# Kernel tuning notes

Measured on AMD Instinct MI355X. Metric: run time of the kernel, lower is better.

The kernel has to match this reference:

```python
import jax, jax.numpy as jnp
import numpy as np

N = 100000   # nodes
E = 3200000  # edges
D = 128      # embedding_dimension


def leaky(x, slope):
    return jnp.where(x >= 0, x, slope * x)


def gat_conv(x, src, dst, lin_w, att_src, att_dst, bias, heads, out_ch):
    """PyG GATConv (concat=True, negative_slope=0.2, add_self_loops handled by caller)."""
    n = x.shape[0]
    h = (x @ lin_w).reshape(n, heads, out_ch)                 # [N,H,C]
    a_s = (h * att_src).sum(-1)                               # [N,H]
    a_d = (h * att_dst).sum(-1)                               # [N,H]
    alpha = leaky(a_s[src] + a_d[dst], 0.2)                   # [E,H]
    # segment softmax over incoming edges of each dst node
    m = jax.ops.segment_max(alpha, dst, num_segments=n)
    ex = jnp.exp(alpha - m[dst])
    s = jax.ops.segment_sum(ex, dst, num_segments=n)
    w = ex / (s[dst] + 1e-16)                                 # [E,H]
    out = jax.ops.segment_sum(h[src] * w[:, :, None], dst, num_segments=n)
    return out.reshape(n, heads * out_ch) + bias


def setup_inputs() -> dict:
    key = jax.random.key(0)
    ks = jax.random.split(key, 32)
    rn = lambda k, s, sc=0.05: jax.random.normal(k, s, dtype=jnp.float32) * sc
    q = D // 4  # 32
    inp = {
        "des": rn(ks[0], (N, 768), 1.0),
        "tweet": rn(ks[1], (N, 768), 1.0),
        "num_prop": rn(ks[2], (N, 6), 1.0),
        "cat_prop": rn(ks[3], (N, 11), 1.0),
        "edge_index": jax.random.randint(ks[4], (2, E), 0, N),
        "edge_type": jax.random.randint(ks[5], (E,), 0, 2),
        # encoder params
        "w_des": rn(ks[6], (768, q)), "b_des": jnp.zeros((q,), jnp.float32),
        "w_tw": rn(ks[7], (768, q)), "b_tw": jnp.zeros((q,), jnp.float32),
        "w_np": rn(ks[8], (6, q)), "b_np": jnp.zeros((q,), jnp.float32),
        "w_cp": rn(ks[9], (11, q)), "b_cp": jnp.zeros((q,), jnp.float32),
        "w_in": rn(ks[10], (D, D)), "b_in": jnp.zeros((D,), jnp.float32),
        # gat1: heads=4, out=32, concat -> 128
        "g1_w": rn(ks[11], (D, 4 * q)), "g1_as": rn(ks[12], (4, q)),
        "g1_ad": rn(ks[13], (4, q)), "g1_b": jnp.zeros((D,), jnp.float32),
        # gat2: heads=1, out=128
        "g2_w": rn(ks[14], (D, D)), "g2_as": rn(ks[15], (1, D)),
        "g2_ad": rn(ks[16], (1, D)), "g2_b": jnp.zeros((D,), jnp.float32),
        # output MLP
        "w_o1": rn(ks[17], (D, D)), "b_o1": jnp.zeros((D,), jnp.float32),
        "w_o2": rn(ks[18], (D, 2)), "b_o2": jnp.zeros((2,), jnp.float32),
    }
    return inp


def reference(des, tweet, num_prop, cat_prop, edge_index, edge_type,
              w_des, b_des, w_tw, b_tw, w_np, b_np, w_cp, b_cp,
              w_in, b_in, g1_w, g1_as, g1_ad, g1_b,
              g2_w, g2_as, g2_ad, g2_b, w_o1, b_o1, w_o2, b_o2):
    # encoders (nn.LeakyReLU default slope = 0.01)
    d = leaky(des @ w_des + b_des, 0.01)
    t = leaky(tweet @ w_tw + b_tw, 0.01)
    n_ = leaky(num_prop @ w_np + b_np, 0.01)
    c = leaky(cat_prop @ w_cp + b_cp, 0.01)
    x = jnp.concatenate([d, t, n_, c], axis=1)          # [N,128]
    x = leaky(x @ w_in + b_in, 0.01)
    # add self-loops (PyG GATConv default add_self_loops=True)
    loop = jnp.arange(N)
    src = jnp.concatenate([edge_index[0], loop])
    dst = jnp.concatenate([edge_index[1], loop])
    x = gat_conv(x, src, dst, g1_w, g1_as, g1_ad, g1_b, 4, D // 4)
    # dropout is identity in eval mode
    x = gat_conv(x, src, dst, g2_w, g2_as, g2_ad, g2_b, 1, D)
    x = leaky(x @ w_o1 + b_o1, 0.01)
    return x @ w_o2 + b_o2                              # [N,2]
```

## Files before the change

kernel.cpp:

```cpp
#include <hip/hip_runtime.h>
#include <hip/hip_bf16.h>

#define DEV_INLINE __device__ __forceinline__

using bf16x8 = __attribute__((ext_vector_type(8))) short;
using f32x4  = __attribute__((ext_vector_type(4))) float;

DEV_INLINE float leaky(float x, float s) { return x >= 0.f ? x : s * x; }
DEV_INLINE float bf2f(unsigned short u) { return __uint_as_float(((unsigned)u) << 16); }
DEV_INLINE unsigned short f2bf(float f) {
  unsigned u = __float_as_uint(f);
  unsigned r = ((u >> 16) & 1u) + 0x7fffu;
  return (unsigned short)((u + r) >> 16);
}
DEV_INLINE float red16(float v) {
  v += __shfl_xor(v, 1, 64); v += __shfl_xor(v, 2, 64);
  v += __shfl_xor(v, 4, 64); v += __shfl_xor(v, 8, 64);
  return v;
}

#define BSHIFT 8
#define NBLK   256

__global__ __launch_bounds__(256) void csr_hist_kernel(
    const int* __restrict__ dst, int* __restrict__ blkcnt, int NB, int E) {
  __shared__ int hist[512];
  int blk = blockIdx.x, t = threadIdx.x;
  for (int i = t; i < NB; i += 256) hist[i] = 0;
  __syncthreads();
  int chunk = (E + NBLK - 1) / NBLK;
  int e0 = blk * chunk;
  int e1 = e0 + chunk; if (e1 > E) e1 = E;
  for (int e = e0 + t; e < e1; e += 256)
    atomicAdd(&hist[dst[e] >> BSHIFT], 1);
  __syncthreads();
  for (int i = t; i < NB; i += 256)
    blkcnt[(size_t)blk * NB + i] = hist[i];
}

__global__ __launch_bounds__(1024) void csr_scan_kernel(
    const int* __restrict__ blkcnt, int* __restrict__ blkoff,
    int* __restrict__ sbkt, int NB) {
  __shared__ int sums[1024];
  int M = NB * NBLK;
  int t = threadIdx.x;
  int chunk = (M + 1023) / 1024;
  int lo = t * chunk;
  int hi = lo + chunk; if (hi > M) hi = M;
  int s = 0;
  for (int q = lo; q < hi; ++q) {
    int b = q >> 8, blk = q & (NBLK - 1);
    s += blkcnt[(size_t)blk * NB + b];
  }
  sums[t] = s;
  __syncthreads();
  for (int off = 1; off < 1024; off <<= 1) {
    int v = (t >= off) ? sums[t - off] : 0;
    __syncthreads();
    sums[t] += v;
    __syncthreads();
  }
  int run = (t == 0) ? 0 : sums[t - 1];
  for (int q = lo; q < hi; ++q) {
    int b = q >> 8, blk = q & (NBLK - 1);
    if (blk == 0) sbkt[b] = run;
    blkoff[(size_t)blk * NB + b] = run;
    run += blkcnt[(size_t)blk * NB + b];
  }
  if (lo < M && hi == M) sbkt[NB] = run;
}

__global__ __launch_bounds__(256) void csr_scatter_kernel(
    const int* __restrict__ src, const int* __restrict__ dst,
    const int* __restrict__ blkoff, int* __restrict__ pairs, int NB, int E) {
  __shared__ int cur[512];
  int blk = blockIdx.x, t = threadIdx.x;
  for (int i = t; i < NB; i += 256) cur[i] = blkoff[(size_t)blk * NB + i];
  __syncthreads();
  int chunk = (E + NBLK - 1) / NBLK;
  int e0 = blk * chunk;
  int e1 = e0 + chunk; if (e1 > E) e1 = E;
  for (int e = e0 + t; e < e1; e += 256) {
    int d = dst[e];
    int pos = atomicAdd(&cur[d >> BSHIFT], 1);
    pairs[pos] = (src[e] << BSHIFT) | (d & 255);
  }
}

__global__ __launch_bounds__(256) void bkt_build_kernel(
    const int* __restrict__ sbkt, const int* __restrict__ pairs,
    int* __restrict__ offs, int* __restrict__ csr, int n_rows, int NB) {
  __shared__ int cnt[256];
  __shared__ int cur[256];
  int b = blockIdx.x, t = threadIdx.x;
  int start = sbkt[b];
  int end   = sbkt[b + 1];
  cnt[t] = 0;
  __syncthreads();
  for (int e = start + t; e < end; e += 256)
    atomicAdd(&cnt[pairs[e] & 255], 1);
  __syncthreads();
  for (int off = 1; off < 256; off <<= 1) {
    int v = (t >= off) ? cnt[t - off] : 0;
    __syncthreads();
    cnt[t] += v;
    __syncthreads();
  }
  int ex = (t == 0) ? 0 : cnt[t - 1];
  cur[t] = start + ex;
  int node = (b << BSHIFT) + t;
  if (node < n_rows) offs[node] = start + ex;
  if (t == 0 && b == NB - 1) offs[n_rows] = end;
  __syncthreads();
  for (int e = start + t; e < end; e += 256) {
    int v = pairs[e];
    int pos = atomicAdd(&cur[v & 255], 1);
    csr[pos] = v >> BSHIFT;
  }
}

__global__ __launch_bounds__(256) void swz_kernel(
    const float* __restrict__ w_des, const float* __restrict__ w_tw,
    const float* __restrict__ w_in, const float* __restrict__ g1_w,
    const float* __restrict__ g2_w, const float* __restrict__ w_o1,
    short* __restrict__ o_des, short* __restrict__ o_tw,
    short* __restrict__ o_in, short* __restrict__ o_g1,
    short* __restrict__ o_g2, short* __restrict__ o_o1) {
  const float* W; short* O; int K, COLS;
  switch (blockIdx.y) {
    case 0: W = w_des; O = o_des; K = 768; COLS = 32; break;
    case 1: W = w_tw;  O = o_tw;  K = 768; COLS = 32; break;
    case 2: W = w_in;  O = o_in;  K = 128; COLS = 128; break;
    case 3: W = g1_w;  O = o_g1;  K = 128; COLS = 128; break;
    case 4: W = g2_w;  O = o_g2;  K = 128; COLS = 128; break;
    default: W = w_o1; O = o_o1;  K = 128; COLS = 128; break;
  }
  int CT = COLS >> 4;
  int t = blockIdx.x * 256 + threadIdx.x;
  int total = (K >> 5) * CT * 64;
  if (t >= total) return;
  int L = t & 63;
  int rest = t >> 6;
  int ct = rest % CT;
  int ks = rest / CT;
  int kbase = ks * 32 + (L >> 4) * 8;
  int col = ct * 16 + (L & 15);
  #pragma unroll
  for (int j = 0; j < 8; ++j)
    O[t * 8 + j] = (short)f2bf(W[(size_t)(kbase + j) * COLS + col]);
}

__global__ __launch_bounds__(256) void enc_mfma_kernel(
    const float* __restrict__ des, const float* __restrict__ tweet,
    const short* __restrict__ wsw_des, const short* __restrict__ wsw_tw,
    const float* __restrict__ b_des, const float* __restrict__ b_tw,
    unsigned short* __restrict__ x0, int n_rows) {
  const float* A; const short* Wsw; const float* bias; int col_off;
  if (blockIdx.y == 0) { A = des;   Wsw = wsw_des; bias = b_des; col_off = 0; }
  else                 { A = tweet; Wsw = wsw_tw;  bias = b_tw;  col_off = 32; }
  int wv = threadIdx.x >> 6, lane = threadIdx.x & 63;
  int row0 = blockIdx.x * 64 + wv * 16;
  int rA = row0 + (lane & 15);
  int rc = rA < n_rows ? rA : (n_rows - 1);
  const float* arow = A + (size_t)rc * 768 + ((lane >> 4) * 8);
  f32x4 acc0 = {0.f, 0.f, 0.f, 0.f}, acc1 = {0.f, 0.f, 0.f, 0.f};

  float4 p0a = *(const float4*)(arow + 0);
  float4 p0b = *(const float4*)(arow + 4);
  float4 p1a = *(const float4*)(arow + 32);
  float4 p1b = *(const float4*)(arow + 36);
  #pragma unroll
  for (int ks = 0; ks < 24; ++ks) {
    float4 c0 = p0a, c1 = p0b;
    p0a = p1a; p0b = p1b;
    if (ks + 2 < 24) {
      p1a = *(const float4*)(arow + (ks + 2) * 32);
      p1b = *(const float4*)(arow + (ks + 2) * 32 + 4);
    }
    bf16x8 af;
    af[0] = (short)f2bf(c0.x); af[1] = (short)f2bf(c0.y);
    af[2] = (short)f2bf(c0.z); af[3] = (short)f2bf(c0.w);
    af[4] = (short)f2bf(c1.x); af[5] = (short)f2bf(c1.y);
    af[6] = (short)f2bf(c1.z); af[7] = (short)f2bf(c1.w);
    bf16x8 b0 = *(const bf16x8*)&Wsw[(size_t)((ks * 2 + 0) * 64 + lane) * 8];
    bf16x8 b1 = *(const bf16x8*)&Wsw[(size_t)((ks * 2 + 1) * 64 + lane) * 8];
    acc0 = __builtin_amdgcn_mfma_f32_16x16x32_bf16(af, b0, acc0, 0, 0, 0);
    acc1 = __builtin_amdgcn_mfma_f32_16x16x32_bf16(af, b1, acc1, 0, 0, 0);
  }
  int quad = lane >> 4, cl = lane & 15;
  #pragma unroll
  for (int r = 0; r < 4; ++r) {
    int row = row0 + quad * 4 + r;
    if (row >= n_rows) continue;
    float v0 = leaky(acc0[r] + bias[cl], 0.01f);
    float v1 = leaky(acc1[r] + bias[16 + cl], 0.01f);
    x0[(size_t)row * 128 + col_off + cl]      = f2bf(v0);
    x0[(size_t)row * 128 + col_off + 16 + cl] = f2bf(v1);
  }
}

__global__ __launch_bounds__(256) void enc_small_kernel(
    const float* __restrict__ np_, const float* __restrict__ cp,
    const float* __restrict__ w_np, const float* __restrict__ w_cp,
    const float* __restrict__ b_np, const float* __restrict__ b_cp,
    unsigned short* __restrict__ x0, int n_rows) {
  int gid = blockIdx.x * 256 + threadIdx.x;
  int node = gid >> 6;
  int c = gid & 63;
  if (node >= n_rows) return;
  float acc; int col;
  if (c < 32) {
    acc = b_np[c];
    #pragma unroll
    for (int k = 0; k < 6; ++k) acc += np_[(size_t)node * 6 + k] * w_np[k * 32 + c];
    col = 64 + c;
  } else {
    int cc = c - 32;
    acc = b_cp[cc];
    #pragma unroll
    for (int k = 0; k < 11; ++k) acc += cp[(size_t)node * 11 + k] * w_cp[k * 32 + cc];
    col = 96 + cc;
  }
  x0[(size_t)node * 128 + col] = f2bf(leaky(acc, 0.01f));
}

__global__ __launch_bounds__(256) void h1_fused_kernel(
    const unsigned short* __restrict__ X, const short* __restrict__ sw_in,
    const float* __restrict__ b_in, const short* __restrict__ sw_g1,
    const float* __restrict__ att_s, const float* __restrict__ att_d,
    unsigned short* __restrict__ H1, float* __restrict__ a_s,
    float* __restrict__ a_d, int n_rows) {
  __shared__ char xt[4 * 4096];
  int wv = threadIdx.x >> 6, lane = threadIdx.x & 63;
  int row0 = blockIdx.x * 64 + wv * 16;
  int rA = row0 + (lane & 15);
  int rc = rA < n_rows ? rA : (n_rows - 1);
  const unsigned short* xr = X + (size_t)rc * 128 + (lane >> 4) * 8;
  int quad = lane >> 4, cl = lane & 15;
  char* xw = xt + wv * 4096;

  f32x4 acc[8] = {};
  #pragma unroll
  for (int ks = 0; ks < 4; ++ks) {
    bf16x8 af = *(const bf16x8*)(xr + ks * 32);
    #pragma unroll
    for (int ct = 0; ct < 8; ++ct) {
      bf16x8 bfr = *(const bf16x8*)&sw_in[(size_t)((ks * 8 + ct) * 64 + lane) * 8];
      acc[ct] = __builtin_amdgcn_mfma_f32_16x16x32_bf16(af, bfr, acc[ct], 0, 0, 0);
    }
  }
  #pragma unroll
  for (int r = 0; r < 4; ++r) {
    int lr = quad * 4 + r;
    #pragma unroll
    for (int ct = 0; ct < 8; ++ct) {
      float v = leaky(acc[ct][r] + b_in[ct * 16 + cl], 0.01f);
      int cb = (ct * 32 + cl * 2) ^ ((lr & 7) << 4);
      *(unsigned short*)(xw + lr * 256 + cb) = f2bf(v);
    }
  }
  f32x4 acc2[8] = {};
  int lr2 = lane & 15;
  #pragma unroll
  for (int ks = 0; ks < 4; ++ks) {
    int cb0 = (((lane >> 4) * 16 + ks * 64)) ^ ((lr2 & 7) << 4);
    bf16x8 af = *(const bf16x8*)(xw + lr2 * 256 + cb0);
    #pragma unroll
    for (int ct = 0; ct < 8; ++ct) {
      bf16x8 bfr = *(const bf16x8*)&sw_g1[(size_t)((ks * 8 + ct) * 64 + lane) * 8];
      acc2[ct] = __builtin_amdgcn_mfma_f32_16x16x32_bf16(af, bfr, acc2[ct], 0, 0, 0);
    }
  }
  float asv[8], adv[8];
  #pragma unroll
  for (int ct = 0; ct < 8; ++ct) {
    int idx = (ct >> 1) * 32 + (ct & 1) * 16 + cl;
    asv[ct] = att_s[idx];
    adv[ct] = att_d[idx];
  }
  #pragma unroll
  for (int r = 0; r < 4; ++r) {
    int row = row0 + quad * 4 + r;
    bool ok = row < n_rows;
    if (ok) {
      #pragma unroll
      for (int ct = 0; ct < 8; ++ct)
        H1[(size_t)row * 128 + ct * 16 + cl] = f2bf(acc2[ct][r]);
    }
    #pragma unroll
    for (int h = 0; h < 4; ++h) {
      float ps = acc2[2 * h][r] * asv[2 * h] + acc2[2 * h + 1][r] * asv[2 * h + 1];
      float pd = acc2[2 * h][r] * adv[2 * h] + acc2[2 * h + 1][r] * adv[2 * h + 1];
      ps = red16(ps); pd = red16(pd);
      if (ok && cl == 0) {
        a_s[(size_t)row * 4 + h] = ps;
        a_d[(size_t)row * 4 + h] = pd;
      }
    }
  }
}

__global__ __launch_bounds__(256) void h2_fused_kernel(
    const unsigned short* __restrict__ X, const short* __restrict__ Wsw,
    const float* __restrict__ att_s, const float* __restrict__ att_d,
    unsigned short* __restrict__ H2, float* __restrict__ a_s,
    float* __restrict__ a_d, int n_rows) {
  int wv = threadIdx.x >> 6, lane = threadIdx.x & 63;
  int row0 = blockIdx.x * 64 + wv * 16;
  int rA = row0 + (lane & 15);
  int rc = rA < n_rows ? rA : (n_rows - 1);
  const unsigned short* xr = X + (size_t)rc * 128 + (lane >> 4) * 8;
  int quad = lane >> 4, cl = lane & 15;
  f32x4 acc[8] = {};
  #pragma unroll
  for (int ks = 0; ks < 4; ++ks) {
    bf16x8 af = *(const bf16x8*)(xr + ks * 32);
    #pragma unroll
    for (int ct = 0; ct < 8; ++ct) {
      bf16x8 bfr = *(const bf16x8*)&Wsw[(size_t)((ks * 8 + ct) * 64 + lane) * 8];
      acc[ct] = __builtin_amdgcn_mfma_f32_16x16x32_bf16(af, bfr, acc[ct], 0, 0, 0);
    }
  }
  float asv[8], adv[8];
  #pragma unroll
  for (int ct = 0; ct < 8; ++ct) {
    asv[ct] = att_s[ct * 16 + cl];
    adv[ct] = att_d[ct * 16 + cl];
  }
  #pragma unroll
  for (int r = 0; r < 4; ++r) {
    int row = row0 + quad * 4 + r;
    bool ok = row < n_rows;
    float ps = 0.f, pd = 0.f;
    #pragma unroll
    for (int ct = 0; ct < 8; ++ct) {
      if (ok) H2[(size_t)row * 128 + ct * 16 + cl] = f2bf(acc[ct][r]);
      ps += acc[ct][r] * asv[ct];
      pd += acc[ct][r] * adv[ct];
    }
    ps = red16(ps); pd = red16(pd);
    if (ok && cl == 0) { a_s[row] = ps; a_d[row] = pd; }
  }
}

__global__ __launch_bounds__(256) void out_fused_kernel(
    const unsigned short* __restrict__ X, const short* __restrict__ Wsw,
    const float* __restrict__ bias, const float* __restrict__ w_o2,
    const float* __restrict__ b_o2, float* __restrict__ out, int n_rows) {
  int wv = threadIdx.x >> 6, lane = threadIdx.x & 63;
  int row0 = blockIdx.x * 64 + wv * 16;
  int rA = row0 + (lane & 15);
  int rc = rA < n_rows ? rA : (n_rows - 1);
  const unsigned short* xr = X + (size_t)rc * 128 + (lane >> 4) * 8;
  int quad = lane >> 4, cl = lane & 15;
  f32x4 acc[8] = {};
  #pragma unroll
  for (int ks = 0; ks < 4; ++ks) {
    bf16x8 af = *(const bf16x8*)(xr + ks * 32);
    #pragma unroll
    for (int ct = 0; ct < 8; ++ct) {
      bf16x8 bfr = *(const bf16x8*)&Wsw[(size_t)((ks * 8 + ct) * 64 + lane) * 8];
      acc[ct] = __builtin_amdgcn_mfma_f32_16x16x32_bf16(af, bfr, acc[ct], 0, 0, 0);
    }
  }
  float w0v[8], w1v[8], bv[8];
  #pragma unroll
  for (int ct = 0; ct < 8; ++ct) {
    int col = ct * 16 + cl;
    w0v[ct] = w_o2[col * 2 + 0];
    w1v[ct] = w_o2[col * 2 + 1];
    bv[ct]  = bias[col];
  }
  float ob0 = b_o2[0], ob1 = b_o2[1];
  #pragma unroll
  for (int r = 0; r < 4; ++r) {
    int row = row0 + quad * 4 + r;
    bool ok = row < n_rows;
    float p0 = 0.f, p1 = 0.f;
    #pragma unroll
    for (int ct = 0; ct < 8; ++ct) {
      float t = leaky(acc[ct][r] + bv[ct], 0.01f);
      p0 += t * w0v[ct];
      p1 += t * w1v[ct];
    }
    p0 = red16(p0); p1 = red16(p1);
    if (ok && cl == 0) {
      out[(size_t)row * 2 + 0] = p0 + ob0;
      out[(size_t)row * 2 + 1] = p1 + ob1;
    }
  }
}

template <int H>
__global__ __launch_bounds__(256) void agg_kernel(
    const ushort2* __restrict__ h2, const float* __restrict__ a_src,
    const float* __restrict__ a_dst, const int* __restrict__ offs,
    const int* __restrict__ csr_src, const float* __restrict__ bias,
    unsigned short* __restrict__ out, int n_rows) {
  int n = (blockIdx.x * 256 + threadIdx.x) >> 6;
  int lane = threadIdx.x & 63;
  if (n >= n_rows) return;
  int c = lane * 2;
  int head = (c * H) >> 7;

  float ad = a_dst[(size_t)n * H + head];
  float m = leaky(a_src[(size_t)n * H + head] + ad, 0.2f);
  float l = 1.0f;
  ushort2 hv = h2[(size_t)n * 64 + lane];
  float acc0 = bf2f(hv.x), acc1 = bf2f(hv.y);

  int e = offs[n], e1 = offs[n + 1];
  for (; e + 4 <= e1; e += 4) {
    int s0 = csr_src[e], s1 = csr_src[e + 1], s2 = csr_src[e + 2], s3 = csr_src[e + 3];
    float a0 = leaky(a_src[(size_t)s0 * H + head] + ad, 0.2f);
    float a1 = leaky(a_src[(size_t)s1 * H + head] + ad, 0.2f);
    float a2 = leaky(a_src[(size_t)s2 * H + head] + ad, 0.2f);
    float a3 = leaky(a_src[(size_t)s3 * H + head] + ad, 0.2f);
    ushort2 g0 = h2[(size_t)s0 * 64 + lane];
    ushort2 g1 = h2[(size_t)s1 * 64 + lane];
    ushort2 g2 = h2[(size_t)s2 * 64 + lane];
    ushort2 g3 = h2[(size_t)s3 * 64 + lane];
    float mn = fmaxf(fmaxf(fmaxf(a0, a1), fmaxf(a2, a3)), m);
    float sc = __expf(m - mn);
    float x0_ = __expf(a0 - mn), x1_ = __expf(a1 - mn);
    float x2_ = __expf(a2 - mn), x3_ = __expf(a3 - mn);
    l = l * sc + x0_ + x1_ + x2_ + x3_;
    acc0 = acc0 * sc + x0_ * bf2f(g0.x) + x1_ * bf2f(g1.x) + x2_ * bf2f(g2.x) + x3_ * bf2f(g3.x);
    acc1 = acc1 * sc + x0_ * bf2f(g0.y) + x1_ * bf2f(g1.y) + x2_ * bf2f(g2.y) + x3_ * bf2f(g3.y);
    m = mn;
  }
  for (; e < e1; ++e) {
    int s = csr_src[e];
    float a = leaky(a_src[(size_t)s * H + head] + ad, 0.2f);
    float mn = fmaxf(m, a);
    float sc = __expf(m - mn), ex = __expf(a - mn);
    ushort2 g = h2[(size_t)s * 64 + lane];
    l = l * sc + ex;
    acc0 = acc0 * sc + ex * bf2f(g.x);
    acc1 = acc1 * sc + ex * bf2f(g.y);
    m = mn;
  }
  float inv = 1.0f / (l + 1e-16f);
  out[(size_t)n * 128 + c]     = f2bf(acc0 * inv + bias[c]);
  out[(size_t)n * 128 + c + 1] = f2bf(acc1 * inv + bias[c + 1]);
}

static inline size_t align256(size_t x) { return (x + 255) & ~(size_t)255; }

extern "C" void kernel_launch(void* const* d_in, const int* in_sizes, int n_in,
                              void* d_out, int out_size, void* d_ws, size_t ws_size,
                              hipStream_t stream) {
  const float* des      = (const float*)d_in[0];
  const float* tweet    = (const float*)d_in[1];
  const float* num_prop = (const float*)d_in[2];
  const float* cat_prop = (const float*)d_in[3];
  const int*   ei       = (const int*)d_in[4];
  const float* w_des = (const float*)d_in[6];
  const float* b_des = (const float*)d_in[7];
  const float* w_tw  = (const float*)d_in[8];
  const float* b_tw  = (const float*)d_in[9];
  const float* w_np  = (const float*)d_in[10];
  const float* b_np  = (const float*)d_in[11];
  const float* w_cp  = (const float*)d_in[12];
  const float* b_cp  = (const float*)d_in[13];
  const float* w_in  = (const float*)d_in[14];
  const float* b_in  = (const float*)d_in[15];
  const float* g1_w  = (const float*)d_in[16];
  const float* g1_as = (const float*)d_in[17];
  const float* g1_ad = (const float*)d_in[18];
  const float* g1_b  = (const float*)d_in[19];
  const float* g2_w  = (const float*)d_in[20];
  const float* g2_as = (const float*)d_in[21];
  const float* g2_ad = (const float*)d_in[22];
  const float* g2_b  = (const float*)d_in[23];
  const float* w_o1  = (const float*)d_in[24];
  const float* b_o1  = (const float*)d_in[25];
  const float* w_o2  = (const float*)d_in[26];
  const float* b_o2  = (const float*)d_in[27];

  const int N = in_sizes[0] / 768;
  const int E = in_sizes[4] / 2;
  const int* src = ei;
  const int* dst = ei + E;

  const int NB = (N + 255) >> BSHIFT;

  char* p = (char*)d_ws;
  unsigned short* bufA = (unsigned short*)p; p += align256((size_t)N * 128 * 2);
  unsigned short* bufB = (unsigned short*)p; p += align256((size_t)N * 128 * 2);
  float* as1 = (float*)p; p += align256((size_t)N * 4 * 4);
  float* ad1 = (float*)p; p += align256((size_t)N * 4 * 4);
  float* as2 = (float*)p; p += align256((size_t)N * 4);
  float* ad2 = (float*)p; p += align256((size_t)N * 4);
  int* offs = (int*)p; p += align256((size_t)(N + 1) * 4);
  int* csr  = (int*)p; p += align256((size_t)E * 4);
  short* sw_des = (short*)p; p += align256(768 * 32 * 2);
  short* sw_tw  = (short*)p; p += align256(768 * 32 * 2);
  short* sw_in  = (short*)p; p += align256(128 * 128 * 2);
  short* sw_g1  = (short*)p; p += align256(128 * 128 * 2);
  short* sw_g2  = (short*)p; p += align256(128 * 128 * 2);
  short* sw_o1  = (short*)p; p += align256(128 * 128 * 2);

  int* pairs = (int*)bufA;
  char* q = (char*)bufB;
  int* blkcnt = (int*)q; q += align256((size_t)NBLK * NB * 4);
  int* blkoff = (int*)q; q += align256((size_t)NBLK * NB * 4);
  int* sbkt   = (int*)q; q += align256((size_t)(NB + 1) * 4);

  dim3 gswz(12, 6);
  swz_kernel<<<gswz, 256, 0, stream>>>(w_des, w_tw, w_in, g1_w, g2_w, w_o1,
                                       sw_des, sw_tw, sw_in, sw_g1, sw_g2, sw_o1);

  csr_hist_kernel<<<NBLK, 256, 0, stream>>>(dst, blkcnt, NB, E);
  csr_scan_kernel<<<1, 1024, 0, stream>>>(blkcnt, blkoff, sbkt, NB);
  csr_scatter_kernel<<<NBLK, 256, 0, stream>>>(src, dst, blkoff, pairs, NB, E);
  bkt_build_kernel<<<NB, 256, 0, stream>>>(sbkt, pairs, offs, csr, N, NB);

  dim3 genc((N + 63) / 64, 2);
  enc_mfma_kernel<<<genc, 256, 0, stream>>>(des, tweet, sw_des, sw_tw, b_des, b_tw, bufA, N);
  enc_small_kernel<<<((size_t)N * 64 + 255) / 256, 256, 0, stream>>>(
      num_prop, cat_prop, w_np, w_cp, b_np, b_cp, bufA, N);

  int gd = (N + 63) / 64;
  int gw = ((size_t)N * 64 + 255) / 256;

  h1_fused_kernel<<<gd, 256, 0, stream>>>(bufA, sw_in, b_in, sw_g1,
                                          g1_as, g1_ad, bufB, as1, ad1, N);
  agg_kernel<4><<<gw, 256, 0, stream>>>((const ushort2*)bufB, as1, ad1, offs, csr, g1_b, bufA, N);

  h2_fused_kernel<<<gd, 256, 0, stream>>>(bufA, sw_g2, g2_as, g2_ad, bufB, as2, ad2, N);
  agg_kernel<1><<<gw, 256, 0, stream>>>((const ushort2*)bufB, as2, ad2, offs, csr, g2_b, bufA, N);

  out_fused_kernel<<<gd, 256, 0, stream>>>(bufA, sw_o1, b_o1, w_o2, b_o2, (float*)d_out, N);
}
```

Baseline: 1.311 ms.

## Stage encoder inputs through swizzled LDS and unroll aggregation by eight

The des/tweet encoder now loads 32 rows per block with fully coalesced float4 reads, converts them to bf16 into an XOR-swizzled shared-memory tile, and has each wave compute one 16x16 output tile from LDS. The old version read strided row segments straight from global memory. The GAT aggregation loop is unrolled from 4 to 8 edges per iteration, so more gathers are in flight and the online-softmax rescaling runs less often. In exchange the encoder uses 48KB of LDS per block, which may limit occupancy, and the wider unroll raises register pressure.

```diff
diff --git a/kernel.cpp b/kernel.cpp
--- a/kernel.cpp
+++ b/kernel.cpp
@@ -150,7 +150,7 @@
     O[t * 8 + j] = (short)f2bf(W[(size_t)(kbase + j) * COLS + col]);
 }
 
-__global__ __launch_bounds__(256) void enc_mfma_kernel(
+__global__ __launch_bounds__(256) void enc_lds_kernel(
     const float* __restrict__ des, const float* __restrict__ tweet,
     const short* __restrict__ wsw_des, const short* __restrict__ wsw_tw,
     const float* __restrict__ b_des, const float* __restrict__ b_tw,
@@ -158,44 +158,44 @@
   const float* A; const short* Wsw; const float* bias; int col_off;
   if (blockIdx.y == 0) { A = des;   Wsw = wsw_des; bias = b_des; col_off = 0; }
   else                 { A = tweet; Wsw = wsw_tw;  bias = b_tw;  col_off = 32; }
-  int wv = threadIdx.x >> 6, lane = threadIdx.x & 63;
-  int row0 = blockIdx.x * 64 + wv * 16;
-  int rA = row0 + (lane & 15);
-  int rc = rA < n_rows ? rA : (n_rows - 1);
-  const float* arow = A + (size_t)rc * 768 + ((lane >> 4) * 8);
-  f32x4 acc0 = {0.f, 0.f, 0.f, 0.f}, acc1 = {0.f, 0.f, 0.f, 0.f};
-
-  float4 p0a = *(const float4*)(arow + 0);
-  float4 p0b = *(const float4*)(arow + 4);
-  float4 p1a = *(const float4*)(arow + 32);
-  float4 p1b = *(const float4*)(arow + 36);
+  __shared__ char xt[32 * 1536];
+  int t = threadIdx.x;
+  int row0 = blockIdx.x * 32;
+
+  #pragma unroll
+  for (int i = 0; i < 24; ++i) {
+    int f = t + i * 256;
+    int row = f / 192;
+    int c4 = f - row * 192;
+    int gr = row0 + row;
+    int grc = gr < n_rows ? gr : (n_rows - 1);
+    float4 v = *(const float4*)(A + (size_t)grc * 768 + c4 * 4);
+    ushort4 b;
+    b.x = f2bf(v.x); b.y = f2bf(v.y); b.z = f2bf(v.z); b.w = f2bf(v.w);
+    *(ushort4*)(xt + row * 1536 + ((c4 * 8) ^ ((row & 7) << 4))) = b;
+  }
+  __syncthreads();
+
+  int wv = t >> 6, lane = t & 63;
+  int rh = wv >> 1, ct = wv & 1;
+  int quad = lane >> 4, cl = lane & 15;
+  int r_loc = rh * 16 + cl;
+  const char* arow = xt + r_loc * 1536;
+  int sw = (r_loc & 7) << 4;
+  f32x4 acc = {0.f, 0.f, 0.f, 0.f};
   #pragma unroll
   for (int ks = 0; ks < 24; ++ks) {
-    float4 c0 = p0a, c1 = p0b;
-    p0a = p1a; p0b = p1b;
-    if (ks + 2 < 24) {
-      p1a = *(const float4*)(arow + (ks + 2) * 32);
-      p1b = *(const float4*)(arow + (ks + 2) * 32 + 4);
-    }
-    bf16x8 af;
-    af[0] = (short)f2bf(c0.x); af[1] = (short)f2bf(c0.y);
-    af[2] = (short)f2bf(c0.z); af[3] = (short)f2bf(c0.w);
-    af[4] = (short)f2bf(c1.x); af[5] = (short)f2bf(c1.y);
-    af[6] = (short)f2bf(c1.z); af[7] = (short)f2bf(c1.w);
-    bf16x8 b0 = *(const bf16x8*)&Wsw[(size_t)((ks * 2 + 0) * 64 + lane) * 8];
-    bf16x8 b1 = *(const bf16x8*)&Wsw[(size_t)((ks * 2 + 1) * 64 + lane) * 8];
-    acc0 = __builtin_amdgcn_mfma_f32_16x16x32_bf16(af, b0, acc0, 0, 0, 0);
-    acc1 = __builtin_amdgcn_mfma_f32_16x16x32_bf16(af, b1, acc1, 0, 0, 0);
-  }
-  int quad = lane >> 4, cl = lane & 15;
+    bf16x8 af = *(const bf16x8*)(arow + ((ks * 64 + quad * 16) ^ sw));
+    bf16x8 bfr = *(const bf16x8*)&Wsw[(size_t)((ks * 2 + ct) * 64 + lane) * 8];
+    acc = __builtin_amdgcn_mfma_f32_16x16x32_bf16(af, bfr, acc, 0, 0, 0);
+  }
+  float bv = bias[ct * 16 + cl];
   #pragma unroll
   for (int r = 0; r < 4; ++r) {
-    int row = row0 + quad * 4 + r;
+    int row = row0 + rh * 16 + quad * 4 + r;
     if (row >= n_rows) continue;
-    float v0 = leaky(acc0[r] + bias[cl], 0.01f);
-    float v1 = leaky(acc1[r] + bias[16 + cl], 0.01f);
-    x0[(size_t)row * 128 + col_off + cl]      = f2bf(v0);
-    x0[(size_t)row * 128 + col_off + 16 + cl] = f2bf(v1);
+    float v = leaky(acc[r] + bv, 0.01f);
+    x0[(size_t)row * 128 + col_off + ct * 16 + cl] = f2bf(v);
   }
 }
 
@@ -410,23 +410,32 @@
   float acc0 = bf2f(hv.x), acc1 = bf2f(hv.y);
 
   int e = offs[n], e1 = offs[n + 1];
-  for (; e + 4 <= e1; e += 4) {
-    int s0 = csr_src[e], s1 = csr_src[e + 1], s2 = csr_src[e + 2], s3 = csr_src[e + 3];
-    float a0 = leaky(a_src[(size_t)s0 * H + head] + ad, 0.2f);
-    float a1 = leaky(a_src[(size_t)s1 * H + head] + ad, 0.2f);
-    float a2 = leaky(a_src[(size_t)s2 * H + head] + ad, 0.2f);
-    float a3 = leaky(a_src[(size_t)s3 * H + head] + ad, 0.2f);
-    ushort2 g0 = h2[(size_t)s0 * 64 + lane];
-    ushort2 g1 = h2[(size_t)s1 * 64 + lane];
-    ushort2 g2 = h2[(size_t)s2 * 64 + lane];
-    ushort2 g3 = h2[(size_t)s3 * 64 + lane];
-    float mn = fmaxf(fmaxf(fmaxf(a0, a1), fmaxf(a2, a3)), m);
+  for (; e + 8 <= e1; e += 8) {
+    int s[8];
+    #pragma unroll
+    for (int i = 0; i < 8; ++i) s[i] = csr_src[e + i];
+    float a[8]; ushort2 g[8];
+    #pragma unroll
+    for (int i = 0; i < 8; ++i) a[i] = leaky(a_src[(size_t)s[i] * H + head] + ad, 0.2f);
+    #pragma unroll
+    for (int i = 0; i < 8; ++i) g[i] = h2[(size_t)s[i] * 64 + lane];
+    float mn = m;
+    #pragma unroll
+    for (int i = 0; i < 8; ++i) mn = fmaxf(mn, a[i]);
     float sc = __expf(m - mn);
-    float x0_ = __expf(a0 - mn), x1_ = __expf(a1 - mn);
-    float x2_ = __expf(a2 - mn), x3_ = __expf(a3 - mn);
-    l = l * sc + x0_ + x1_ + x2_ + x3_;
-    acc0 = acc0 * sc + x0_ * bf2f(g0.x) + x1_ * bf2f(g1.x) + x2_ * bf2f(g2.x) + x3_ * bf2f(g3.x);
-    acc1 = acc1 * sc + x0_ * bf2f(g0.y) + x1_ * bf2f(g1.y) + x2_ * bf2f(g2.y) + x3_ * bf2f(g3.y);
+    float x[8];
+    #pragma unroll
+    for (int i = 0; i < 8; ++i) x[i] = __expf(a[i] - mn);
+    float ls = 0.f, p0 = 0.f, p1 = 0.f;
+    #pragma unroll
+    for (int i = 0; i < 8; ++i) {
+      ls += x[i];
+      p0 += x[i] * bf2f(g[i].x);
+      p1 += x[i] * bf2f(g[i].y);
+    }
+    l = l * sc + ls;
+    acc0 = acc0 * sc + p0;
+    acc1 = acc1 * sc + p1;
     m = mn;
   }
   for (; e < e1; ++e) {
@@ -516,8 +525,8 @@
   csr_scatter_kernel<<<NBLK, 256, 0, stream>>>(src, dst, blkoff, pairs, NB, E);
   bkt_build_kernel<<<NB, 256, 0, stream>>>(sbkt, pairs, offs, csr, N, NB);
 
-  dim3 genc((N + 63) / 64, 2);
-  enc_mfma_kernel<<<genc, 256, 0, stream>>>(des, tweet, sw_des, sw_tw, b_des, b_tw, bufA, N);
+  dim3 genc((N + 31) / 32, 2);
+  enc_lds_kernel<<<genc, 256, 0, stream>>>(des, tweet, sw_des, sw_tw, b_des, b_tw, bufA, N);
   enc_small_kernel<<<((size_t)N * 64 + 255) / 256, 256, 0, stream>>>(
       num_prop, cat_prop, w_np, w_cp, b_np, b_cp, bufA, N);
 
```

After: 1.284 ms. 2.1% less time.
